# Kernel optimization log

Hardware: AMD Instinct MI355X
Metric: run time of the kernel (lower is better)

## Reference

```python
import jax, jax.numpy as jnp
import numpy as np

jax.config.update("jax_enable_x64", True)

N = 256          # nFeatures
B = 64           # batch
C = 10.0         # capacity
DATA_SIZE = 256.0
EPS = 1e-4       # QP regularization strength (Q = EPS * I)
ITERS = 20       # fixed primal-dual interior-point iterations
SIGMA = 0.1      # centering parameter


def build_Gh(indices_male):
    """Constraints for fair_mode=1: sum x <= C, 0 <= x <= 1, fairness band on male subset."""
    m = indices_male.astype(jnp.float64)
    I = jnp.eye(N, dtype=jnp.float64)
    G = jnp.concatenate([jnp.ones((1, N)), -I, I, m[None, :], -m[None, :]], axis=0)  # [2N+3, N]
    rhs_fair = C * m.sum() / DATA_SIZE
    h = jnp.concatenate([
        jnp.array([C]),
        jnp.zeros(N, dtype=jnp.float64),
        jnp.ones(N, dtype=jnp.float64),
        jnp.array([rhs_fair + 1.0]),
        jnp.array([-rhs_fair]),
    ])  # [2N+3]
    return G, h


def solve_qp(p, G, h):
    """Batched PDIPM: min 0.5*EPS*x'x + p'x  s.t. G x <= h.  p: [B, N]."""
    nb, m = p.shape[0], G.shape[0]
    x = jnp.zeros_like(p)
    s = jnp.ones((nb, m), dtype=p.dtype)
    z = jnp.ones((nb, m), dtype=p.dtype)
    I_n = jnp.eye(N, dtype=p.dtype)

    def maxstep(v, dv):
        r = jnp.where(dv < 0, -v / dv, jnp.inf)
        return jnp.min(r, axis=1)

    def step(carry, _):
        x, s, z = carry
        mu = jnp.mean(s * z, axis=1, keepdims=True)
        rx = EPS * x + p + z @ G              # Q x + p + G^T z, [B, N]
        rs = s + x @ G.T - h                  # primal residual (G x + s - h)
        rc = s * z - SIGMA * mu               # complementarity residual
        d = z / s                             # [B, m]
        # Schur complement: Q + G^T diag(d) G, batched over B
        M = EPS * I_n + jnp.einsum('bm,mi,mj->bij', d, G, G)
        rhs = -(rx + ((-rc + z * rs) / s) @ G)
        dx = jnp.linalg.solve(M, rhs[..., None])[..., 0]
        ds = -rs - dx @ G.T
        dz = (-rc - z * ds) / s
        alpha = jnp.minimum(1.0, 0.99 * jnp.minimum(maxstep(s, ds), maxstep(z, dz)))[:, None]
        return (x + alpha * dx, s + alpha * ds, z + alpha * dz), None

    (x, s, z), _ = jax.lax.scan(step, (x, s, z), None, length=ITERS)
    return x


def setup_inputs() -> dict:
    key = jax.random.key(0)
    k1, k2 = jax.random.split(key)
    x = jax.random.normal(k1, (B, N), dtype=jnp.float32)
    indices_male = jax.random.randint(k2, (N,), 0, 2)
    return {"x": x, "indices_male": indices_male}


def reference(x, indices_male):
    G, h = build_Gh(indices_male)
    p = -x.astype(jnp.float64)                # QPFunction(Q, -inputs, ...)
    sol = solve_qp(p, G, h)
    return sol.astype(jnp.float32)
```

## Files before the change

kernel.cpp:

```cpp
#include <hip/hip_runtime.h>
#include <math.h>

#define NF 256
#define NB 64
#define M_CON 515
static constexpr double EPS_Q  = 1e-4;
static constexpr double SIGMA  = 0.1;
static constexpr double CAPC   = 10.0;
static constexpr int    ITERS  = 20;

__device__ __forceinline__ double drcp(double x) {
    double r = __builtin_amdgcn_rcp(x);
    r = fma(r, fma(-x, r, 1.0), r);
    return r;
}
__device__ __forceinline__ double drcp_fast(double x) {
    return __builtin_amdgcn_rcp(x);
}

template <int CTRL>
__device__ __forceinline__ double dpp_d(double v) {
    const int lo = __builtin_amdgcn_update_dpp(0, __double2loint(v), CTRL, 0xF, 0xF, true);
    const int hi = __builtin_amdgcn_update_dpp(0, __double2hiint(v), CTRL, 0xF, 0xF, true);
    return __hiloint2double(hi, lo);
}
__device__ __forceinline__ double bcast63(double v) {
    const int lo = __builtin_amdgcn_readlane(__double2loint(v), 63);
    const int hi = __builtin_amdgcn_readlane(__double2hiint(v), 63);
    return __hiloint2double(hi, lo);
}
__device__ __forceinline__ double wave_red_sum(double v) {
    v += dpp_d<0x121>(v);
    v += dpp_d<0x122>(v);
    v += dpp_d<0x124>(v);
    v += dpp_d<0x128>(v);
    v += dpp_d<0x142>(v);
    v += dpp_d<0x143>(v);
    return bcast63(v);
}
__device__ __forceinline__ double wave_red_max_nn(double v) {
    v = fmax(v, dpp_d<0x121>(v));
    v = fmax(v, dpp_d<0x122>(v));
    v = fmax(v, dpp_d<0x124>(v));
    v = fmax(v, dpp_d<0x128>(v));
    v = fmax(v, dpp_d<0x142>(v));
    v = fmax(v, dpp_d<0x143>(v));
    return bcast63(v);
}

__global__ __launch_bounds__(64)
void pdipm_kernel(const float* __restrict__ xin,
                  const int* __restrict__ male,
                  float* __restrict__ out) {
    const int b = blockIdx.x;
    const int lane = threadIdx.x;

    double e[4], mf[4], x[4];
    double s_lo[4], s_hi[4], z_lo[4], z_hi[4];
    double rs_lo[4], rs_hi[4];
    double msum_p = 0.0;
    #pragma unroll
    for (int k = 0; k < 4; ++k) {
        const int f = lane + 64 * k;
        e[k]  = (double)xin[b * NF + f];
        mf[k] = (double)male[f];
        msum_p += mf[k];
        x[k] = 0.0;
        s_lo[k] = 1.0; s_hi[k] = 1.0;
        z_lo[k] = 1.0; z_hi[k] = 1.0;
        rs_lo[k] = 1.0;
        rs_hi[k] = 0.0;
    }
    const double nm = wave_red_sum(msum_p);
    const double rhs_fair = CAPC * nm * (1.0 / 256.0);

    double s0 = 1.0, z0 = 1.0, sA = 1.0, zA = 1.0, sB = 1.0, zB = 1.0;
    double rs0 = 1.0 - CAPC;
    double rsA = -rhs_fair;
    double rsB = 1.0 + rhs_fair;
    double musum = (double)M_CON;

    for (int it = 0; it < ITERS; ++it) {
        const double smu = SIGMA * musum * (1.0 / (double)M_CON);

        const double i_s0 = drcp(s0), i_sA = drcp(sA), i_sB = drcp(sB);
        const double i_z0 = drcp_fast(z0), i_zA = drcp_fast(zA), i_zB = drcp_fast(zB);
        const double d0 = z0 * i_s0, dA = zA * i_sA, dB = zB * i_sB;
        const double beta  = d0 * rs0 + smu * i_s0;
        const double gamma = (dA * rsA + smu * i_sA) - (dB * rsB + smu * i_sB);
        const double ia  = drcp(d0);
        const double ibb = drcp(dA + dB);
        const double g0 = fma(smu, i_s0, -z0);
        const double gA = fma(smu, i_sA, -zA);
        const double gB = fma(smu, i_sB, -zB);

        double invD[4], y[4], i_sl[4], i_sh[4], i_zl[4], i_zh[4];
        double dl[4], dh[4], gl[4], gh[4];
        #pragma unroll
        for (int k = 0; k < 4; ++k) {
            const double prod  = s_lo[k] * s_hi[k];
            const double denom = fma(EPS_Q, prod,
                                     fma(z_lo[k], s_hi[k], z_hi[k] * s_lo[k]));
            const double R = drcp(denom);
            invD[k] = prod * R;
            const double Nr = fma(e[k], prod,
                              fma(z_lo[k] * rs_lo[k], s_hi[k],
                              fma(-(z_hi[k] * rs_hi[k]), s_lo[k],
                                  smu * (s_hi[k] - s_lo[k]))));
            y[k] = Nr * R;
            i_sl[k] = drcp(s_lo[k]);
            i_sh[k] = drcp(s_hi[k]);
            i_zl[k] = drcp_fast(z_lo[k]);
            i_zh[k] = drcp_fast(z_hi[k]);
            dl[k] = z_lo[k] * i_sl[k];
            dh[k] = z_hi[k] * i_sh[k];
            gl[k] = fma(smu, i_sl[k], -z_lo[k]);
            gh[k] = fma(smu, i_sh[k], -z_hi[k]);
        }
        const double s11 = wave_red_sum((invD[0] + invD[1]) + (invD[2] + invD[3]));
        const double s12 = wave_red_sum((mf[0] * invD[0] + mf[1] * invD[1])
                                      + (mf[2] * invD[2] + mf[3] * invD[3]));
        const double t1  = wave_red_sum((y[0] + y[1]) + (y[2] + y[3]));
        const double t2  = wave_red_sum((mf[0] * y[0] + mf[1] * y[1])
                                      + (mf[2] * y[2] + mf[3] * y[3]));

        const double k11 = ia + s11;
        const double k22 = ibb + s12;
        const double i_det = drcp(k11 * k22 - s12 * s12);
        const double c1 = (k22 * t1 - s12 * t2) * i_det;
        const double c2 = (k11 * t2 - s12 * t1) * i_det;
        const double a1 =  ia * k22 * i_det;
        const double a2 = -ia * s12 * i_det;
        const double b1 = -ibb * s12 * i_det;
        const double b2 =  ibb * k11 * i_det;
        const double C1 = c1 + beta * a1 + gamma * b1;
        const double C2 = c2 + beta * a2 + gamma * b2;
        const double C1pC2 = C1 + C2;

        const double Sdx  = t1 - C1 * s11 - C2 * s12;
        const double Smdx = t2 - C1pC2 * s12;
        const double ds0 = -rs0 - Sdx;
        const double dsA = -rsA - Smdx;
        const double dsB = -rsB + Smdx;
        const double dz0 = fma(-d0, ds0, g0);
        const double dzA = fma(-dA, dsA, gA);
        const double dzB = fma(-dB, dsB, gB);

        double rmax_p = fmax(fmax(-ds0 * i_s0, -dz0 * i_z0),
                       fmax(fmax(-dsA * i_sA, -dzA * i_zA),
                            fmax(-dsB * i_sB, -dzB * i_zB)));
        rmax_p = fmax(rmax_p, 0.0);
        const double dsdz_scal = ds0 * dz0 + dsA * dzA + dsB * dzB;
        double dsdz_p = (lane == 0) ? dsdz_scal : 0.0;
        double dx[4], ds_l[4], ds_h[4], dz_l[4], dz_h[4];
        #pragma unroll
        for (int k = 0; k < 4; ++k) {
            const double C12 = (mf[k] != 0.0) ? C1pC2 : C1;
            dx[k] = fma(-invD[k], C12, y[k]);
            ds_l[k] = dx[k] - rs_lo[k];
            ds_h[k] = -dx[k] - rs_hi[k];
            dz_l[k] = fma(-dl[k], ds_l[k], gl[k]);
            dz_h[k] = fma(-dh[k], ds_h[k], gh[k]);
            dsdz_p += ds_l[k] * dz_l[k] + ds_h[k] * dz_h[k];
            rmax_p = fmax(rmax_p,
                     fmax(fmax(-ds_l[k] * i_sl[k], -ds_h[k] * i_sh[k]),
                          fmax(-dz_l[k] * i_zl[k], -dz_h[k] * i_zh[k])));
        }
        const double Sdsdz = wave_red_sum(dsdz_p);
        const double rmax  = wave_red_max_nn(rmax_p);

        const double alpha = fmin(1.0, 0.99 * drcp_fast(fmax(rmax, 0.99)));
        const double omA = 1.0 - alpha;

        #pragma unroll
        for (int k = 0; k < 4; ++k) {
            const double adx = alpha * dx[k];
            x[k] += adx;
            e[k] = fma(-EPS_Q, adx, e[k]);
            s_lo[k] = fma(alpha, ds_l[k], s_lo[k]);
            s_hi[k] = fma(alpha, ds_h[k], s_hi[k]);
            z_lo[k] = fma(alpha, dz_l[k], z_lo[k]);
            z_hi[k] = fma(alpha, dz_h[k], z_hi[k]);
            rs_lo[k] *= omA;
            rs_hi[k] *= omA;
        }
        s0 = fma(alpha, ds0, s0); z0 = fma(alpha, dz0, z0);
        sA = fma(alpha, dsA, sA); zA = fma(alpha, dzA, zA);
        sB = fma(alpha, dsB, sB); zB = fma(alpha, dzB, zB);
        rs0 *= omA; rsA *= omA; rsB *= omA;
        musum = musum * (1.0 - alpha * (1.0 - SIGMA)) + alpha * alpha * Sdsdz;
    }

    #pragma unroll
    for (int k = 0; k < 4; ++k)
        out[b * NF + lane + 64 * k] = (float)x[k];
}

extern "C" void kernel_launch(void* const* d_in, const int* in_sizes, int n_in,
                              void* d_out, int out_size, void* d_ws, size_t ws_size,
                              hipStream_t stream) {
    const float* xin  = (const float*)d_in[0];
    const int*   male = (const int*)d_in[1];
    float* out = (float*)d_out;
    pdipm_kernel<<<NB, 64, 0, stream>>>(xin, male, out);
}
```

Baseline: 73.51 us.

## Compute step-length ratios and max reduction in fp32, fold beta/gamma into RHS

The step-size ratio computation and its wave max-reduction move from double to single precision, using fp32 reciprocals for z and a 32-bit DPP reduction. The beta/gamma correction terms are folded into the per-feature numerator, which simplifies the 2x2 solve to a single Newton-corrected reciprocal. The male mask becomes a boolean select instead of double multiplies. This cuts fp64 ALU work and cross-lane traffic, at the risk of a slightly different alpha because of fp32 rounding.

```diff
diff --git a/kernel.cpp b/kernel.cpp
--- a/kernel.cpp
+++ b/kernel.cpp
@@ -14,9 +14,6 @@
     r = fma(r, fma(-x, r, 1.0), r);
     return r;
 }
-__device__ __forceinline__ double drcp_fast(double x) {
-    return __builtin_amdgcn_rcp(x);
-}
 
 template <int CTRL>
 __device__ __forceinline__ double dpp_d(double v) {
@@ -24,10 +21,18 @@
     const int hi = __builtin_amdgcn_update_dpp(0, __double2hiint(v), CTRL, 0xF, 0xF, true);
     return __hiloint2double(hi, lo);
 }
+template <int CTRL>
+__device__ __forceinline__ float dpp_f(float v) {
+    return __int_as_float(
+        __builtin_amdgcn_update_dpp(0, __float_as_int(v), CTRL, 0xF, 0xF, true));
+}
 __device__ __forceinline__ double bcast63(double v) {
     const int lo = __builtin_amdgcn_readlane(__double2loint(v), 63);
     const int hi = __builtin_amdgcn_readlane(__double2hiint(v), 63);
     return __hiloint2double(hi, lo);
+}
+__device__ __forceinline__ float bcast63f(float v) {
+    return __int_as_float(__builtin_amdgcn_readlane(__float_as_int(v), 63));
 }
 __device__ __forceinline__ double wave_red_sum(double v) {
     v += dpp_d<0x121>(v);
@@ -38,14 +43,14 @@
     v += dpp_d<0x143>(v);
     return bcast63(v);
 }
-__device__ __forceinline__ double wave_red_max_nn(double v) {
-    v = fmax(v, dpp_d<0x121>(v));
-    v = fmax(v, dpp_d<0x122>(v));
-    v = fmax(v, dpp_d<0x124>(v));
-    v = fmax(v, dpp_d<0x128>(v));
-    v = fmax(v, dpp_d<0x142>(v));
-    v = fmax(v, dpp_d<0x143>(v));
-    return bcast63(v);
+__device__ __forceinline__ float wave_red_maxf_nn(float v) {
+    v = fmaxf(v, dpp_f<0x121>(v));
+    v = fmaxf(v, dpp_f<0x122>(v));
+    v = fmaxf(v, dpp_f<0x124>(v));
+    v = fmaxf(v, dpp_f<0x128>(v));
+    v = fmaxf(v, dpp_f<0x142>(v));
+    v = fmaxf(v, dpp_f<0x143>(v));
+    return bcast63f(v);
 }
 
 __global__ __launch_bounds__(64)
@@ -55,7 +60,8 @@
     const int b = blockIdx.x;
     const int lane = threadIdx.x;
 
-    double e[4], mf[4], x[4];
+    double e[4], x[4];
+    bool mb[4];
     double s_lo[4], s_hi[4], z_lo[4], z_hi[4];
     double rs_lo[4], rs_hi[4];
     double msum_p = 0.0;
@@ -63,8 +69,9 @@
     for (int k = 0; k < 4; ++k) {
         const int f = lane + 64 * k;
         e[k]  = (double)xin[b * NF + f];
-        mf[k] = (double)male[f];
-        msum_p += mf[k];
+        const int m = male[f];
+        mb[k] = (m != 0);
+        msum_p += (double)m;
         x[k] = 0.0;
         s_lo[k] = 1.0; s_hi[k] = 1.0;
         z_lo[k] = 1.0; z_hi[k] = 1.0;
@@ -84,17 +91,17 @@
         const double smu = SIGMA * musum * (1.0 / (double)M_CON);
 
         const double i_s0 = drcp(s0), i_sA = drcp(sA), i_sB = drcp(sB);
-        const double i_z0 = drcp_fast(z0), i_zA = drcp_fast(zA), i_zB = drcp_fast(zB);
         const double d0 = z0 * i_s0, dA = zA * i_sA, dB = zB * i_sB;
         const double beta  = d0 * rs0 + smu * i_s0;
         const double gamma = (dA * rsA + smu * i_sA) - (dB * rsB + smu * i_sB);
+        const double bpg = beta + gamma;
         const double ia  = drcp(d0);
         const double ibb = drcp(dA + dB);
         const double g0 = fma(smu, i_s0, -z0);
         const double gA = fma(smu, i_sA, -zA);
         const double gB = fma(smu, i_sB, -zB);
 
-        double invD[4], y[4], i_sl[4], i_sh[4], i_zl[4], i_zh[4];
+        double invD[4], y[4], i_sl[4], i_sh[4];
         double dl[4], dh[4], gl[4], gh[4];
         #pragma unroll
         for (int k = 0; k < 4; ++k) {
@@ -103,38 +110,34 @@
                                      fma(z_lo[k], s_hi[k], z_hi[k] * s_lo[k]));
             const double R = drcp(denom);
             invD[k] = prod * R;
-            const double Nr = fma(e[k], prod,
-                              fma(z_lo[k] * rs_lo[k], s_hi[k],
-                              fma(-(z_hi[k] * rs_hi[k]), s_lo[k],
-                                  smu * (s_hi[k] - s_lo[k]))));
+            const double w = mb[k] ? bpg : beta;
+            const double Nr0 = fma(e[k], prod,
+                               fma(z_lo[k] * rs_lo[k], s_hi[k],
+                               fma(-(z_hi[k] * rs_hi[k]), s_lo[k],
+                                   smu * (s_hi[k] - s_lo[k]))));
+            const double Nr = fma(-w, prod, Nr0);
             y[k] = Nr * R;
             i_sl[k] = drcp(s_lo[k]);
             i_sh[k] = drcp(s_hi[k]);
-            i_zl[k] = drcp_fast(z_lo[k]);
-            i_zh[k] = drcp_fast(z_hi[k]);
             dl[k] = z_lo[k] * i_sl[k];
             dh[k] = z_hi[k] * i_sh[k];
             gl[k] = fma(smu, i_sl[k], -z_lo[k]);
             gh[k] = fma(smu, i_sh[k], -z_hi[k]);
         }
         const double s11 = wave_red_sum((invD[0] + invD[1]) + (invD[2] + invD[3]));
-        const double s12 = wave_red_sum((mf[0] * invD[0] + mf[1] * invD[1])
-                                      + (mf[2] * invD[2] + mf[3] * invD[3]));
+        const double s12 = wave_red_sum((mb[0] ? invD[0] : 0.0) + (mb[1] ? invD[1] : 0.0)
+                                      + ((mb[2] ? invD[2] : 0.0) + (mb[3] ? invD[3] : 0.0)));
         const double t1  = wave_red_sum((y[0] + y[1]) + (y[2] + y[3]));
-        const double t2  = wave_red_sum((mf[0] * y[0] + mf[1] * y[1])
-                                      + (mf[2] * y[2] + mf[3] * y[3]));
+        const double t2  = wave_red_sum((mb[0] ? y[0] : 0.0) + (mb[1] ? y[1] : 0.0)
+                                      + ((mb[2] ? y[2] : 0.0) + (mb[3] ? y[3] : 0.0)));
 
         const double k11 = ia + s11;
         const double k22 = ibb + s12;
-        const double i_det = drcp(k11 * k22 - s12 * s12);
-        const double c1 = (k22 * t1 - s12 * t2) * i_det;
-        const double c2 = (k11 * t2 - s12 * t1) * i_det;
-        const double a1 =  ia * k22 * i_det;
-        const double a2 = -ia * s12 * i_det;
-        const double b1 = -ibb * s12 * i_det;
-        const double b2 =  ibb * k11 * i_det;
-        const double C1 = c1 + beta * a1 + gamma * b1;
-        const double C2 = c2 + beta * a2 + gamma * b2;
+        const double den2 = k11 * k22 - s12 * s12;
+        const double r2 = __builtin_amdgcn_rcp(den2);
+        const double corr = fma(-den2, r2, 2.0);
+        const double C1 = ((k22 * t1 - s12 * t2) * r2) * corr;
+        const double C2 = ((k11 * t2 - s12 * t1) * r2) * corr;
         const double C1pC2 = C1 + C2;
 
         const double Sdx  = t1 - C1 * s11 - C2 * s12;
@@ -146,30 +149,33 @@
         const double dzA = fma(-dA, dsA, gA);
         const double dzB = fma(-dB, dsB, gB);
 
-        double rmax_p = fmax(fmax(-ds0 * i_s0, -dz0 * i_z0),
-                       fmax(fmax(-dsA * i_sA, -dzA * i_zA),
-                            fmax(-dsB * i_sB, -dzB * i_zB)));
-        rmax_p = fmax(rmax_p, 0.0);
-        const double dsdz_scal = ds0 * dz0 + dsA * dzA + dsB * dzB;
-        double dsdz_p = (lane == 0) ? dsdz_scal : 0.0;
+        float rmax_p = fmaxf(
+            fmaxf(fmaxf((float)(-ds0 * i_s0), -(float)dz0 * __builtin_amdgcn_rcpf((float)z0)),
+                  fmaxf((float)(-dsA * i_sA), -(float)dzA * __builtin_amdgcn_rcpf((float)zA))),
+            fmaxf(fmaxf((float)(-dsB * i_sB), -(float)dzB * __builtin_amdgcn_rcpf((float)zB)),
+                  0.0f));
+        double dsdz_p = (lane == 0) ? (ds0 * dz0 + dsA * dzA + dsB * dzB) : 0.0;
         double dx[4], ds_l[4], ds_h[4], dz_l[4], dz_h[4];
         #pragma unroll
         for (int k = 0; k < 4; ++k) {
-            const double C12 = (mf[k] != 0.0) ? C1pC2 : C1;
+            const double C12 = mb[k] ? C1pC2 : C1;
             dx[k] = fma(-invD[k], C12, y[k]);
             ds_l[k] = dx[k] - rs_lo[k];
             ds_h[k] = -dx[k] - rs_hi[k];
             dz_l[k] = fma(-dl[k], ds_l[k], gl[k]);
             dz_h[k] = fma(-dh[k], ds_h[k], gh[k]);
             dsdz_p += ds_l[k] * dz_l[k] + ds_h[k] * dz_h[k];
-            rmax_p = fmax(rmax_p,
-                     fmax(fmax(-ds_l[k] * i_sl[k], -ds_h[k] * i_sh[k]),
-                          fmax(-dz_l[k] * i_zl[k], -dz_h[k] * i_zh[k])));
+            const float qs = fmaxf((float)(-ds_l[k] * i_sl[k]),
+                                   (float)(-ds_h[k] * i_sh[k]));
+            const float qzl = -(float)dz_l[k] * __builtin_amdgcn_rcpf((float)z_lo[k]);
+            const float qzh = -(float)dz_h[k] * __builtin_amdgcn_rcpf((float)z_hi[k]);
+            rmax_p = fmaxf(rmax_p, fmaxf(qs, fmaxf(qzl, qzh)));
         }
         const double Sdsdz = wave_red_sum(dsdz_p);
-        const double rmax  = wave_red_max_nn(rmax_p);
-
-        const double alpha = fmin(1.0, 0.99 * drcp_fast(fmax(rmax, 0.99)));
+        const float  rmax  = wave_red_maxf_nn(rmax_p);
+
+        const float  alphaf = fminf(1.0f, 0.99f * __builtin_amdgcn_rcpf(fmaxf(rmax, 0.99f)));
+        const double alpha  = (double)alphaf;
         const double omA = 1.0 - alpha;
 
         #pragma unroll
```

After: 74.96 us. No clear change (+2.0%).
